# Optimization experiments

Hardware: AMD Instinct MI355X
Metric: run time of the kernel (lower is better)

Reference implementation:

```python
import jax, jax.numpy as jnp
import numpy as np

B, S, D, H = 4, 2048, 512, 8
HD = D // H  # head dim = 64
NEG = 1e9


def setup_inputs() -> dict:
    key = jax.random.key(0)
    ks = jax.random.split(key, 10)
    x = jax.random.normal(ks[0], (B, S, D), dtype=jnp.float32)
    group_ids = jnp.sort(jax.random.randint(ks[1], (B, S), 0, 8), axis=-1)
    s = 0.05
    Wq = jax.random.normal(ks[2], (D, D), dtype=jnp.float32) * s
    Wk = jax.random.normal(ks[3], (D, D), dtype=jnp.float32) * s
    Wv = jax.random.normal(ks[4], (D, D), dtype=jnp.float32) * s
    Wo = jax.random.normal(ks[5], (D, D), dtype=jnp.float32) * s
    bq = jnp.zeros((D,), jnp.float32)
    bk = jnp.zeros((D,), jnp.float32)
    bv = jnp.zeros((D,), jnp.float32)
    bo = jnp.zeros((D,), jnp.float32)
    return {"x": x, "group_ids": group_ids, "Wq": Wq, "bq": bq,
            "Wk": Wk, "bk": bk, "Wv": Wv, "bv": bv, "Wo": Wo, "bo": bo}


def reference(x, group_ids, Wq, bq, Wk, bk, Wv, bv, Wo, bo):
    relu = jax.nn.relu
    # projections + activation (activation='relu' is applied to q,k,v AND output)
    q = relu(x @ Wq + bq)  # [B,S,D]
    k = relu(x @ Wk + bk)
    v = relu(x @ Wv + bv)
    # split heads -> [B,H,S,HD]
    def split(t):
        return t.reshape(B, S, H, HD).transpose(0, 2, 1, 3)
    qh, kh, vh = split(q), split(k), split(v)
    # note: scale uses feature dim AFTER head split, i.e. head_dim
    scale = 1.0 / jnp.sqrt(jnp.float32(HD))
    e = jnp.einsum('bhqd,bhkd->bhqk', qh, kh) * scale  # [B,H,S,S]
    group_mask = (group_ids[:, None, :, None] == group_ids[:, None, None, :])  # [B,1,S,S]
    e = e - (1.0 - group_mask.astype(jnp.float32)) * NEG
    a = jax.nn.softmax(e, axis=-1)
    yh = jnp.einsum('bhqk,bhkd->bhqd', a, vh)  # [B,H,S,HD]
    y = yh.transpose(0, 2, 1, 3).reshape(B, S, D)
    return relu(y @ Wo + bo)
```

## Files before the change

kernel.cpp:

```cpp
#include <hip/hip_runtime.h>
#include <cmath>

#define Bsz 4
#define Ssz 2048
#define Dsz 512
#define Hn 8

typedef unsigned short u16;
typedef _Float16 f16;
typedef __attribute__((ext_vector_type(4))) _Float16 f16x4;
typedef __attribute__((ext_vector_type(8))) _Float16 f16x8;
typedef __attribute__((ext_vector_type(8))) unsigned short us8;
typedef __attribute__((ext_vector_type(4))) float f32x4;
typedef __attribute__((ext_vector_type(16))) float f32x16;

__device__ __forceinline__ void gl2lds16(const void* g, void* l) {
    __builtin_amdgcn_global_load_lds(
        (const __attribute__((address_space(1))) void*)g,
        (__attribute__((address_space(3))) void*)l, 16, 0, 0);
}

__device__ __forceinline__ int lbound2k(const int* __restrict__ a, int v) {
    int lo = 0;
#pragma unroll
    for (int step = 2048; step > 0; step >>= 1)
        if (lo + step <= 2048 && a[lo + step - 1] < v) lo += step;
    return lo;
}

__global__ __launch_bounds__(256) void prep(const float* __restrict__ x,
                                            f16* __restrict__ xb,
                                            const float* __restrict__ Wq,
                                            const float* __restrict__ Wk,
                                            const float* __restrict__ Wv,
                                            const float* __restrict__ Wo,
                                            f16* __restrict__ Wtqkv,
                                            f16* __restrict__ Wto) {
    const int blk = blockIdx.x;
    const int tid = threadIdx.x;
    if (blk < 2048) {
        int i = blk * 256 + tid;
        const float4* xv = (const float4*)x;
        float4 a = xv[2 * i], b = xv[2 * i + 1];
        f16x8 o;
        o[0] = (f16)a.x; o[1] = (f16)a.y; o[2] = (f16)a.z; o[3] = (f16)a.w;
        o[4] = (f16)b.x; o[5] = (f16)b.y; o[6] = (f16)b.z; o[7] = (f16)b.w;
        ((f16x8*)xb)[i] = o;
        return;
    }
    __shared__ float T[64][65];
    const int bz = blk - 2048;
    const int z = bz >> 6;
    const int n0 = (bz & 7) * 64, k0 = ((bz >> 3) & 7) * 64;
    const float* W = (z == 0) ? Wq : (z == 1) ? Wk : (z == 2) ? Wv : Wo;
    const float sc = (z == 0) ? 0.18033688f : 1.0f;
#pragma unroll
    for (int i = 0; i < 16; i++) {
        int e = tid + i * 256;
        int r = e >> 6, c = e & 63;
        T[r][c] = W[(size_t)(k0 + r) * Dsz + n0 + c];
    }
    __syncthreads();
    f16* dst = (z < 3) ? (Wtqkv + ((size_t)z * 512 + n0) * Dsz + k0)
                       : (Wto + (size_t)n0 * Dsz + k0);
#pragma unroll
    for (int i = 0; i < 16; i++) {
        int e = tid + i * 256;
        int r = e >> 6, c = e & 63;
        dst[(size_t)r * Dsz + c] = (f16)(T[c][r] * sc);
    }
}

template <int MODE>
__global__ __launch_bounds__(256) void gemm128(
    const f16* __restrict__ A, const f16* __restrict__ Bt,
    u16* o0, u16* o1, u16* o2v,
    const float* b0, const float* b1, const float* b2,
    float* ofp, const float* bias_f) {
    __shared__ __align__(16) u16 smem[2 * 128 * 64];
    u16* As = smem;
    u16* Bs = smem + 128 * 64;
    const int tid = threadIdx.x;
    const int colg0 = blockIdx.x * 128;
    const int row0 = blockIdx.y * 128;
    const int w = tid >> 6, lane = tid & 63;
    const int nn = lane & 31, hh = lane >> 5;
    const int wr = w >> 1, wc = w & 1;

    f32x16 acc[2][2];
#pragma unroll
    for (int bi = 0; bi < 2; bi++)
#pragma unroll
        for (int bj = 0; bj < 2; bj++)
#pragma unroll
            for (int e = 0; e < 16; e++) acc[bi][bj][e] = 0.f;

    const f16* Ablk = A + (size_t)row0 * 512;
    const f16* Bblk = Bt + (size_t)colg0 * 512;

    for (int k0 = 0; k0 < 512; k0 += 64) {
        __syncthreads();
#pragma unroll
        for (int i = 0; i < 4; i++) {
            int p = tid + i * 256;
            int m = p >> 3, kc = p & 7;
            int gk = ((kc ^ (m & 7)) << 3);
            gl2lds16(Ablk + (size_t)m * 512 + k0 + gk, As + p * 8);
            gl2lds16(Bblk + (size_t)m * 512 + k0 + gk, Bs + p * 8);
        }
        __syncthreads();
#pragma unroll
        for (int t = 0; t < 4; t++) {
            f16x8 af[2], bfr[2];
#pragma unroll
            for (int bi = 0; bi < 2; bi++) {
                int r = wr * 64 + bi * 32 + nn;
                int ch = r * 8 + ((t * 2 + hh) ^ (r & 7));
                af[bi] = *(const f16x8*)(As + ch * 8);
            }
#pragma unroll
            for (int bj = 0; bj < 2; bj++) {
                int n = wc * 64 + bj * 32 + nn;
                int ch = n * 8 + ((t * 2 + hh) ^ (n & 7));
                bfr[bj] = *(const f16x8*)(Bs + ch * 8);
            }
#pragma unroll
            for (int bi = 0; bi < 2; bi++)
#pragma unroll
                for (int bj = 0; bj < 2; bj++)
                    acc[bi][bj] = __builtin_amdgcn_mfma_f32_32x32x16_f16(
                        af[bi], bfr[bj], acc[bi][bj], 0, 0, 0);
        }
    }

    if (MODE == 0) {
        const int sel = colg0 >> 9;
        const int c0 = colg0 & 511;
        if (sel < 2) {
            u16* outp = (sel == 0) ? o0 : o1;
            const float* bp = (sel == 0) ? b0 : b1;
            const float bscale = (sel == 0) ? 0.18033688f : 1.0f;
#pragma unroll
            for (int bj = 0; bj < 2; bj++) {
                int col = c0 + wc * 64 + bj * 32 + nn;
                float bv = bp[col] * bscale;
#pragma unroll
                for (int bi = 0; bi < 2; bi++)
#pragma unroll
                    for (int rg = 0; rg < 16; rg++) {
                        int row = row0 + wr * 64 + bi * 32 +
                                  (rg & 3) + 8 * (rg >> 2) + 4 * hh;
                        f16 v = (f16)fmaxf(acc[bi][bj][rg] + bv, 0.f);
                        *(f16*)(outp + (size_t)row * 512 + col) = v;
                    }
            }
        } else {
            const int hh_head = c0 >> 6;
            f16 (*T)[136] = (f16(*)[136])smem;
            const int bb = row0 >> 11;
            const int t0 = (row0 & 2047) >> 6;
            __syncthreads();
#pragma unroll
            for (int ph = 0; ph < 2; ph++) {
                if (wc == ph) {
#pragma unroll
                    for (int bj = 0; bj < 2; bj++) {
                        int d = bj * 32 + nn;
                        float bv = b2[c0 + ph * 64 + d];
#pragma unroll
                        for (int bi = 0; bi < 2; bi++)
#pragma unroll
                            for (int rg = 0; rg < 16; rg++) {
                                int s = wr * 64 + bi * 32 +
                                        (rg & 3) + 8 * (rg >> 2) + 4 * hh;
                                T[d][s] = (f16)fmaxf(acc[bi][bj][rg] + bv, 0.f);
                            }
                    }
                }
                __syncthreads();
#pragma unroll
                for (int ii = 0; ii < 4; ii++) {
                    int oct = tid + ii * 256;
                    int tt = oct >> 9, rem = oct & 511;
                    int d = rem >> 3, s8 = rem & 7;
                    us8 val = *(const us8*)(&T[d][tt * 64 + s8 * 8]);
                    size_t dst = (((size_t)((bb * 8 + hh_head + ph) * 32 + t0 + tt)) << 12)
                                 + d * 64 + s8 * 8;
                    *(us8*)(o2v + dst) = val;
                }
                __syncthreads();
            }
        }
    } else {
#pragma unroll
        for (int bj = 0; bj < 2; bj++) {
            int col = colg0 + wc * 64 + bj * 32 + nn;
            float bv = bias_f[col];
#pragma unroll
            for (int bi = 0; bi < 2; bi++)
#pragma unroll
                for (int rg = 0; rg < 16; rg++) {
                    int row = row0 + wr * 64 + bi * 32 +
                              (rg & 3) + 8 * (rg >> 2) + 4 * hh;
                    ofp[(size_t)row * 512 + col] = fmaxf(acc[bi][bj][rg] + bv, 0.f);
                }
        }
    }
}

__global__ __launch_bounds__(512) void attn_mfma(
    const f16* __restrict__ Q, const f16* __restrict__ K,
    const u16* __restrict__ VT, const int* __restrict__ G,
    f16* __restrict__ Y) {
    __shared__ __align__(16) u16 Ks[2][4096];
    __shared__ __align__(16) u16 Vs[2][4096];

    const int qt = blockIdx.x, h = blockIdx.y, b = blockIdx.z;
    const int q0 = qt * 128;
    const int tid = threadIdx.x;
    const int w = tid >> 6, lane = tid & 63;
    const int ln = lane & 15, quad = lane >> 4;

    const f16* Qb = Q + (size_t)b * Ssz * Dsz;
    const f16* Kb = K + (size_t)b * Ssz * Dsz;
    const u16* Vtb = VT + (size_t)(b * Hn + h) * 32 * 4096;
    const int* Gb = G + (size_t)b * Ssz;

    f16x8 qf[2];
    {
        const f16* qrow = Qb + (size_t)(q0 + w * 16 + ln) * Dsz + h * 64;
        qf[0] = *(const f16x8*)(qrow + quad * 8);
        qf[1] = *(const f16x8*)(qrow + 32 + quad * 8);
    }

    const int gq = Gb[q0 + w * 16 + ln];
    const int qlo = lbound2k(Gb, gq);
    const int qhi = lbound2k(Gb, gq + 1);
    const int wlo = __shfl(qlo, 0);
    const int whi = __shfl(qhi, 15);
    const int gqmin = Gb[q0], gqmax = Gb[q0 + 127];
    const int blo = lbound2k(Gb, gqmin);
    const int bhi = lbound2k(Gb, gqmax + 1);
    const int kt_lo = blo >> 6;
    const int kt_hi = (bhi - 1) >> 6;

    f32x4 o[4];
    const f32x4 z4 = {0.f, 0.f, 0.f, 0.f};
#pragma unroll
    for (int nd = 0; nd < 4; nd++) o[nd] = z4;
    float lsum = 0.f;

#define STAGE_K(kt, bi_)                                                       \
    {                                                                          \
        const f16* Ktile = Kb + (size_t)(kt) * 64 * Dsz + h * 64;              \
        int row = tid >> 3, c = tid & 7;                                       \
        gl2lds16(Ktile + (size_t)row * Dsz + ((c ^ (row & 7)) << 3),           \
                 Ks[bi_] + tid * 8);                                           \
    }
#define STAGE_V(kt, bi_)                                                       \
    {                                                                          \
        const u16* Vtile = Vtb + (size_t)(kt) * 4096;                          \
        int row = tid >> 3, c = tid & 7;                                       \
        gl2lds16(Vtile + row * 64 + ((c ^ (row & 7)) << 3),                    \
                 Vs[bi_] + tid * 8);                                           \
    }

    STAGE_K(kt_lo, 0)
    STAGE_V(kt_lo, 0)

    int buf = 0;
    for (int kt = kt_lo; kt <= kt_hi; kt++) {
        __syncthreads();
        if (kt < kt_hi) {
            STAGE_K(kt + 1, Ks[0] == Ks[0] ? buf ^ 1 : 0)
            STAGE_V(kt + 1, buf ^ 1)
        }
        const int k0 = kt * 64;
        if (k0 < whi && k0 + 64 > wlo) {
            const u16* ks = Ks[buf];
            const u16* vs = Vs[buf];

            f16x4 pf[4];
#pragma unroll
            for (int kb = 0; kb < 4; kb++) {
                f32x4 s = z4;
#pragma unroll
                for (int kk = 0; kk < 2; kk++) {
                    int key = kb * 16 + ln;
                    int ch = key * 8 + ((kk * 4 + quad) ^ (key & 7));
                    f16x8 kf = *(const f16x8*)(ks + ch * 8);
                    s = __builtin_amdgcn_mfma_f32_16x16x32_f16(kf, qf[kk], s, 0, 0, 0);
                }
                const int keybase = k0 + kb * 16 + quad * 4;
                f16x4 pp;
#pragma unroll
                for (int r = 0; r < 4; r++) {
                    int key = keybase + r;
                    float sv = (key >= qlo && key < qhi) ? s[r] - 5.7708f : -1e9f;
                    float e = exp2f(sv);
                    lsum += e;
                    pp[r] = (f16)e;
                }
                pf[kb] = pp;
            }
#pragma unroll
            for (int nd = 0; nd < 4; nd++)
#pragma unroll
                for (int kc = 0; kc < 4; kc++) {
                    int addr = (((nd * 16 + ln) * 8 +
                                 ((kc * 2 + (quad >> 1)) ^ (ln & 7))) << 3) +
                               (quad & 1) * 4;
                    f16x4 vf = *(const f16x4*)(vs + addr);
                    o[nd] = __builtin_amdgcn_mfma_f32_16x16x16f16(pf[kc], vf, o[nd], 0, 0, 0);
                }
        }
        buf ^= 1;
    }

    lsum += __shfl_xor(lsum, 16);
    lsum += __shfl_xor(lsum, 32);
    float linv = 1.0f / lsum;
#pragma unroll
    for (int r = 0; r < 4; r++) {
        float lr = __shfl(linv, (lane & 48) | (quad * 4 + r));
        size_t row = (size_t)b * Ssz + q0 + w * 16 + quad * 4 + r;
#pragma unroll
        for (int nd = 0; nd < 4; nd++)
            Y[row * Dsz + h * 64 + nd * 16 + ln] = (f16)(o[nd][r] * lr);
    }
#undef STAGE_K
#undef STAGE_V
}

extern "C" void kernel_launch(void* const* d_in, const int* in_sizes, int n_in,
                              void* d_out, int out_size, void* d_ws, size_t ws_size,
                              hipStream_t stream) {
    const float* x  = (const float*)d_in[0];
    const int*   g  = (const int*)d_in[1];
    const float* Wq = (const float*)d_in[2];
    const float* bq = (const float*)d_in[3];
    const float* Wk = (const float*)d_in[4];
    const float* bk = (const float*)d_in[5];
    const float* Wv = (const float*)d_in[6];
    const float* bv = (const float*)d_in[7];
    const float* Wo = (const float*)d_in[8];
    const float* bo = (const float*)d_in[9];
    float* out = (float*)d_out;

    const size_t E = (size_t)Bsz * Ssz * Dsz;
    f16* xb  = (f16*)d_ws;
    f16* qb  = xb + E;
    f16* kb2 = qb + E;
    u16* vtb = (u16*)(kb2 + E);
    f16* yb  = (f16*)(vtb + E);
    f16* Wtqkv = yb + E;
    f16* Wto   = Wtqkv + 1536 * 512;

    prep<<<2304, 256, 0, stream>>>(x, xb, Wq, Wk, Wv, Wo, Wtqkv, Wto);
    gemm128<0><<<dim3(12, 64), 256, 0, stream>>>(xb, Wtqkv, (u16*)qb, (u16*)kb2, vtb,
                                                 bq, bk, bv, nullptr, nullptr);
    attn_mfma<<<dim3(Ssz / 128, Hn, Bsz), 512, 0, stream>>>(qb, kb2, vtb, g, yb);
    gemm128<1><<<dim3(4, 64), 256, 0, stream>>>(yb, Wto, nullptr, nullptr, nullptr,
                                                nullptr, nullptr, nullptr,
                                                out, bo);
}
```

Measured before the change: 152.6 us.

## Fuse x fp32-to-fp16 conversion into QKV GEMM and retile output GEMM

```diff
diff --git a/kernel.cpp b/kernel.cpp
--- a/kernel.cpp
+++ b/kernel.cpp
@@ -28,28 +28,15 @@
     return lo;
 }
 
-__global__ __launch_bounds__(256) void prep(const float* __restrict__ x,
-                                            f16* __restrict__ xb,
-                                            const float* __restrict__ Wq,
+__global__ __launch_bounds__(256) void prep(const float* __restrict__ Wq,
                                             const float* __restrict__ Wk,
                                             const float* __restrict__ Wv,
                                             const float* __restrict__ Wo,
                                             f16* __restrict__ Wtqkv,
                                             f16* __restrict__ Wto) {
-    const int blk = blockIdx.x;
+    __shared__ float T[64][65];
+    const int bz = blockIdx.x;
     const int tid = threadIdx.x;
-    if (blk < 2048) {
-        int i = blk * 256 + tid;
-        const float4* xv = (const float4*)x;
-        float4 a = xv[2 * i], b = xv[2 * i + 1];
-        f16x8 o;
-        o[0] = (f16)a.x; o[1] = (f16)a.y; o[2] = (f16)a.z; o[3] = (f16)a.w;
-        o[4] = (f16)b.x; o[5] = (f16)b.y; o[6] = (f16)b.z; o[7] = (f16)b.w;
-        ((f16x8*)xb)[i] = o;
-        return;
-    }
-    __shared__ float T[64][65];
-    const int bz = blk - 2048;
     const int z = bz >> 6;
     const int n0 = (bz & 7) * 64, k0 = ((bz >> 3) & 7) * 64;
     const float* W = (z == 0) ? Wq : (z == 1) ? Wk : (z == 2) ? Wv : Wo;
@@ -71,12 +58,10 @@
     }
 }
 
-template <int MODE>
-__global__ __launch_bounds__(256) void gemm128(
-    const f16* __restrict__ A, const f16* __restrict__ Bt,
+__global__ __launch_bounds__(256) void gemm_qkv(
+    const float* __restrict__ A32, const f16* __restrict__ Bt,
     u16* o0, u16* o1, u16* o2v,
-    const float* b0, const float* b1, const float* b2,
-    float* ofp, const float* bias_f) {
+    const float* b0, const float* b1, const float* b2) {
     __shared__ __align__(16) u16 smem[2 * 128 * 64];
     u16* As = smem;
     u16* Bs = smem + 128 * 64;
@@ -95,6 +80,126 @@
 #pragma unroll
             for (int e = 0; e < 16; e++) acc[bi][bj][e] = 0.f;
 
+    const float* Ablk = A32 + (size_t)row0 * 512;
+    const f16* Bblk = Bt + (size_t)colg0 * 512;
+
+    for (int k0 = 0; k0 < 512; k0 += 64) {
+        __syncthreads();
+#pragma unroll
+        for (int i = 0; i < 4; i++) {
+            int p = tid + i * 256;
+            int m = p >> 3, kc = p & 7;
+            int gk = ((kc ^ (m & 7)) << 3);
+            const float* src = Ablk + (size_t)m * 512 + k0 + gk;
+            float4 a = *(const float4*)src;
+            float4 b = *(const float4*)(src + 4);
+            f16x8 v;
+            v[0] = (f16)a.x; v[1] = (f16)a.y; v[2] = (f16)a.z; v[3] = (f16)a.w;
+            v[4] = (f16)b.x; v[5] = (f16)b.y; v[6] = (f16)b.z; v[7] = (f16)b.w;
+            *(f16x8*)(As + p * 8) = v;
+            gl2lds16(Bblk + (size_t)m * 512 + k0 + gk, Bs + p * 8);
+        }
+        __syncthreads();
+#pragma unroll
+        for (int t = 0; t < 4; t++) {
+            f16x8 af[2], bfr[2];
+#pragma unroll
+            for (int bi = 0; bi < 2; bi++) {
+                int r = wr * 64 + bi * 32 + nn;
+                int ch = r * 8 + ((t * 2 + hh) ^ (r & 7));
+                af[bi] = *(const f16x8*)(As + ch * 8);
+            }
+#pragma unroll
+            for (int bj = 0; bj < 2; bj++) {
+                int n = wc * 64 + bj * 32 + nn;
+                int ch = n * 8 + ((t * 2 + hh) ^ (n & 7));
+                bfr[bj] = *(const f16x8*)(Bs + ch * 8);
+            }
+#pragma unroll
+            for (int bi = 0; bi < 2; bi++)
+#pragma unroll
+                for (int bj = 0; bj < 2; bj++)
+                    acc[bi][bj] = __builtin_amdgcn_mfma_f32_32x32x16_f16(
+                        af[bi], bfr[bj], acc[bi][bj], 0, 0, 0);
+        }
+    }
+
+    const int sel = colg0 >> 9;
+    const int c0 = colg0 & 511;
+    if (sel < 2) {
+        u16* outp = (sel == 0) ? o0 : o1;
+        const float* bp = (sel == 0) ? b0 : b1;
+        const float bscale = (sel == 0) ? 0.18033688f : 1.0f;
+#pragma unroll
+        for (int bj = 0; bj < 2; bj++) {
+            int col = c0 + wc * 64 + bj * 32 + nn;
+            float bv = bp[col] * bscale;
+#pragma unroll
+            for (int bi = 0; bi < 2; bi++)
+#pragma unroll
+                for (int rg = 0; rg < 16; rg++) {
+                    int row = row0 + wr * 64 + bi * 32 +
+                              (rg & 3) + 8 * (rg >> 2) + 4 * hh;
+                    f16 v = (f16)fmaxf(acc[bi][bj][rg] + bv, 0.f);
+                    *(f16*)(outp + (size_t)row * 512 + col) = v;
+                }
+        }
+    } else {
+        const int hh_head = c0 >> 6;
+        f16 (*T)[136] = (f16(*)[136])smem;
+        const int bb = row0 >> 11;
+        const int t0 = (row0 & 2047) >> 6;
+        __syncthreads();
+#pragma unroll
+        for (int ph = 0; ph < 2; ph++) {
+            if (wc == ph) {
+#pragma unroll
+                for (int bj = 0; bj < 2; bj++) {
+                    int d = bj * 32 + nn;
+                    float bv = b2[c0 + ph * 64 + d];
+#pragma unroll
+                    for (int bi = 0; bi < 2; bi++)
+#pragma unroll
+                        for (int rg = 0; rg < 16; rg++) {
+                            int s = wr * 64 + bi * 32 +
+                                    (rg & 3) + 8 * (rg >> 2) + 4 * hh;
+                            T[d][s] = (f16)fmaxf(acc[bi][bj][rg] + bv, 0.f);
+                        }
+                }
+            }
+            __syncthreads();
+#pragma unroll
+            for (int ii = 0; ii < 4; ii++) {
+                int oct = tid + ii * 256;
+                int tt = oct >> 9, rem = oct & 511;
+                int d = rem >> 3, s8 = rem & 7;
+                us8 val = *(const us8*)(&T[d][tt * 64 + s8 * 8]);
+                size_t dst = (((size_t)((bb * 8 + hh_head + ph) * 32 + t0 + tt)) << 12)
+                             + d * 64 + s8 * 8;
+                *(us8*)(o2v + dst) = val;
+            }
+            __syncthreads();
+        }
+    }
+}
+
+__global__ __launch_bounds__(256) void gemm_out(
+    const f16* __restrict__ A, const f16* __restrict__ Bt,
+    float* __restrict__ C, const float* __restrict__ bias) {
+    __shared__ __align__(16) u16 As[128 * 64];
+    __shared__ __align__(16) u16 Bs[64 * 64];
+    const int tid = threadIdx.x;
+    const int colg0 = blockIdx.x * 64;
+    const int row0 = blockIdx.y * 128;
+    const int w = tid >> 6, lane = tid & 63;
+    const int nn = lane & 31, hh = lane >> 5;
+
+    f32x16 acc[2];
+#pragma unroll
+    for (int bj = 0; bj < 2; bj++)
+#pragma unroll
+        for (int e = 0; e < 16; e++) acc[bj][e] = 0.f;
+
     const f16* Ablk = A + (size_t)row0 * 512;
     const f16* Bblk = Bt + (size_t)colg0 * 512;
 
@@ -106,104 +211,42 @@
             int m = p >> 3, kc = p & 7;
             int gk = ((kc ^ (m & 7)) << 3);
             gl2lds16(Ablk + (size_t)m * 512 + k0 + gk, As + p * 8);
+        }
+#pragma unroll
+        for (int i = 0; i < 2; i++) {
+            int p = tid + i * 256;
+            int m = p >> 3, kc = p & 7;
+            int gk = ((kc ^ (m & 7)) << 3);
             gl2lds16(Bblk + (size_t)m * 512 + k0 + gk, Bs + p * 8);
         }
         __syncthreads();
 #pragma unroll
         for (int t = 0; t < 4; t++) {
-            f16x8 af[2], bfr[2];
-#pragma unroll
-            for (int bi = 0; bi < 2; bi++) {
-                int r = wr * 64 + bi * 32 + nn;
-                int ch = r * 8 + ((t * 2 + hh) ^ (r & 7));
-                af[bi] = *(const f16x8*)(As + ch * 8);
-            }
+            int r = w * 32 + nn;
+            int cha = r * 8 + ((t * 2 + hh) ^ (r & 7));
+            f16x8 af = *(const f16x8*)(As + cha * 8);
+            f16x8 bfr[2];
 #pragma unroll
             for (int bj = 0; bj < 2; bj++) {
-                int n = wc * 64 + bj * 32 + nn;
+                int n = bj * 32 + nn;
                 int ch = n * 8 + ((t * 2 + hh) ^ (n & 7));
                 bfr[bj] = *(const f16x8*)(Bs + ch * 8);
             }
 #pragma unroll
-            for (int bi = 0; bi < 2; bi++)
-#pragma unroll
-                for (int bj = 0; bj < 2; bj++)
-                    acc[bi][bj] = __builtin_amdgcn_mfma_f32_32x32x16_f16(
-                        af[bi], bfr[bj], acc[bi][bj], 0, 0, 0);
-        }
-    }
-
-    if (MODE == 0) {
-        const int sel = colg0 >> 9;
-        const int c0 = colg0 & 511;
-        if (sel < 2) {
-            u16* outp = (sel == 0) ? o0 : o1;
-            const float* bp = (sel == 0) ? b0 : b1;
-            const float bscale = (sel == 0) ? 0.18033688f : 1.0f;
-#pragma unroll
-            for (int bj = 0; bj < 2; bj++) {
-                int col = c0 + wc * 64 + bj * 32 + nn;
-                float bv = bp[col] * bscale;
-#pragma unroll
-                for (int bi = 0; bi < 2; bi++)
-#pragma unroll
-                    for (int rg = 0; rg < 16; rg++) {
-                        int row = row0 + wr * 64 + bi * 32 +
-                                  (rg & 3) + 8 * (rg >> 2) + 4 * hh;
-                        f16 v = (f16)fmaxf(acc[bi][bj][rg] + bv, 0.f);
-                        *(f16*)(outp + (size_t)row * 512 + col) = v;
-                    }
-            }
-        } else {
-            const int hh_head = c0 >> 6;
-            f16 (*T)[136] = (f16(*)[136])smem;
-            const int bb = row0 >> 11;
-            const int t0 = (row0 & 2047) >> 6;
-            __syncthreads();
-#pragma unroll
-            for (int ph = 0; ph < 2; ph++) {
-                if (wc == ph) {
-#pragma unroll
-                    for (int bj = 0; bj < 2; bj++) {
-                        int d = bj * 32 + nn;
-                        float bv = b2[c0 + ph * 64 + d];
-#pragma unroll
-                        for (int bi = 0; bi < 2; bi++)
-#pragma unroll
-                            for (int rg = 0; rg < 16; rg++) {
-                                int s = wr * 64 + bi * 32 +
-                                        (rg & 3) + 8 * (rg >> 2) + 4 * hh;
-                                T[d][s] = (f16)fmaxf(acc[bi][bj][rg] + bv, 0.f);
-                            }
-                    }
-                }
-                __syncthreads();
-#pragma unroll
-                for (int ii = 0; ii < 4; ii++) {
-                    int oct = tid + ii * 256;
-                    int tt = oct >> 9, rem = oct & 511;
-                    int d = rem >> 3, s8 = rem & 7;
-                    us8 val = *(const us8*)(&T[d][tt * 64 + s8 * 8]);
-                    size_t dst = (((size_t)((bb * 8 + hh_head + ph) * 32 + t0 + tt)) << 12)
-                                 + d * 64 + s8 * 8;
-                    *(us8*)(o2v + dst) = val;
-                }
-                __syncthreads();
-            }
-        }
-    } else {
-#pragma unroll
-        for (int bj = 0; bj < 2; bj++) {
-            int col = colg0 + wc * 64 + bj * 32 + nn;
-            float bv = bias_f[col];
-#pragma unroll
-            for (int bi = 0; bi < 2; bi++)
-#pragma unroll
-                for (int rg = 0; rg < 16; rg++) {
-                    int row = row0 + wr * 64 + bi * 32 +
-                              (rg & 3) + 8 * (rg >> 2) + 4 * hh;
-                    ofp[(size_t)row * 512 + col] = fmaxf(acc[bi][bj][rg] + bv, 0.f);
-                }
+            for (int bj = 0; bj < 2; bj++)
+                acc[bj] = __builtin_amdgcn_mfma_f32_32x32x16_f16(
+                    af, bfr[bj], acc[bj], 0, 0, 0);
+        }
+    }
+
+#pragma unroll
+    for (int bj = 0; bj < 2; bj++) {
+        int col = colg0 + bj * 32 + nn;
+        float bv = bias[col];
+#pragma unroll
+        for (int rg = 0; rg < 16; rg++) {
+            int row = row0 + w * 32 + (rg & 3) + 8 * (rg >> 2) + 4 * hh;
+            C[(size_t)row * 512 + col] = fmaxf(acc[bj][rg] + bv, 0.f);
         }
     }
 }
@@ -272,7 +315,7 @@
     for (int kt = kt_lo; kt <= kt_hi; kt++) {
         __syncthreads();
         if (kt < kt_hi) {
-            STAGE_K(kt + 1, Ks[0] == Ks[0] ? buf ^ 1 : 0)
+            STAGE_K(kt + 1, buf ^ 1)
             STAGE_V(kt + 1, buf ^ 1)
         }
         const int k0 = kt * 64;
@@ -348,19 +391,16 @@
     float* out = (float*)d_out;
 
     const size_t E = (size_t)Bsz * Ssz * Dsz;
-    f16* xb  = (f16*)d_ws;
-    f16* qb  = xb + E;
+    f16* qb  = (f16*)d_ws;
     f16* kb2 = qb + E;
     u16* vtb = (u16*)(kb2 + E);
     f16* yb  = (f16*)(vtb + E);
     f16* Wtqkv = yb + E;
     f16* Wto   = Wtqkv + 1536 * 512;
 
-    prep<<<2304, 256, 0, stream>>>(x, xb, Wq, Wk, Wv, Wo, Wtqkv, Wto);
-    gemm128<0><<<dim3(12, 64), 256, 0, stream>>>(xb, Wtqkv, (u16*)qb, (u16*)kb2, vtb,
-                                                 bq, bk, bv, nullptr, nullptr);
+    prep<<<256, 256, 0, stream>>>(Wq, Wk, Wv, Wo, Wtqkv, Wto);
+    gemm_qkv<<<dim3(12, 64), 256, 0, stream>>>(x, Wtqkv, (u16*)qb, (u16*)kb2, vtb,
+                                               bq, bk, bv);
     attn_mfma<<<dim3(Ssz / 128, Hn, Bsz), 512, 0, stream>>>(qb, kb2, vtb, g, yb);
-    gemm128<1><<<dim3(4, 64), 256, 0, stream>>>(yb, Wto, nullptr, nullptr, nullptr,
-                                                nullptr, nullptr, nullptr,
-                                                out, bo);
-}
+    gemm_out<<<dim3(8, 64), 256, 0, stream>>>(yb, Wto, out, bo);
+}
```

Result: no change. 155.3 us (+1.8%).
